# Optimization experiments

Hardware: AMD Instinct MI355X
Metric: run time of the kernel (lower is better)

Reference implementation:

```python
import jax, jax.numpy as jnp
import numpy as np

EPS = 1e-07


def _splat_one(inp, idx4, w4, n):
    # inp: [C1, N] weighted features for one batch element
    # idx4: [4, N] int32 flat target indices (clipped)
    # w4:  [4, N] bilinear weights (zeroed where out of bounds)
    out = jnp.zeros((inp.shape[0], n), dtype=inp.dtype)
    for k in range(4):
        out = out.at[:, idx4[k]].add(inp * w4[k])
    return out


def _softsplat(x, flow, metric):
    B, C, H, W = x.shape
    N = H * W
    m = jnp.exp(metric)                      # [B,1,H,W]
    inp = jnp.concatenate([x * m, m], axis=1)  # [B,C+1,H,W]

    gy, gx = jnp.meshgrid(jnp.arange(H, dtype=x.dtype),
                          jnp.arange(W, dtype=x.dtype), indexing='ij')
    tx = gx[None] + flow[:, 0]               # [B,H,W] target x
    ty = gy[None] + flow[:, 1]               # [B,H,W] target y

    x0f = jnp.floor(tx)
    y0f = jnp.floor(ty)
    x0 = x0f.astype(jnp.int32)
    y0 = y0f.astype(jnp.int32)
    x1 = x0 + 1
    y1 = y0 + 1

    fx = tx - x0f                            # frac parts
    fy = ty - y0f
    # bilinear weights for (x0,y0),(x1,y0),(x0,y1),(x1,y1)
    w = jnp.stack([(1 - fx) * (1 - fy),
                   fx * (1 - fy),
                   (1 - fx) * fy,
                   fx * fy], axis=1)          # [B,4,H,W]
    xs = jnp.stack([x0, x1, x0, x1], axis=1)  # [B,4,H,W]
    ys = jnp.stack([y0, y0, y1, y1], axis=1)

    valid = (xs >= 0) & (xs < W) & (ys >= 0) & (ys < H)
    w = jnp.where(valid, w, 0.0).reshape(B, 4, N)
    idx = (jnp.clip(ys, 0, H - 1) * W + jnp.clip(xs, 0, W - 1)).reshape(B, 4, N)

    inp_flat = inp.reshape(B, C + 1, N)
    out = jax.vmap(lambda i, ix, ww: _splat_one(i, ix, ww, N))(inp_flat, idx, w)
    out = out.reshape(B, C + 1, H, W)
    return out[:, :-1] / (out[:, -1:] + EPS)


def setup_inputs() -> dict:
    key = jax.random.key(0)
    k1, k2, k3 = jax.random.split(key, 3)
    x = jax.random.normal(k1, (8, 64, 256, 448), dtype=jnp.float32)
    flow = jax.random.normal(k2, (8, 2, 256, 448), dtype=jnp.float32)
    metric = jax.random.normal(k3, (8, 1, 256, 448), dtype=jnp.float32)
    return {"x": x, "flow": flow, "metric": metric}


def reference(x, flow, metric):
    return _softsplat(x, flow, metric)
```

## Files before the change

kernel.cpp:

```cpp
#include <hip/hip_runtime.h>

#define EPS 1e-7f

constexpr int B = 8, C = 64, H = 256, W = 448;
constexpr int N = H * W;
constexpr int P = B * N;

constexpr int TS  = 16;
constexpr int NT  = 256;
constexpr int RW  = 8;
constexpr int WIN = 32;
constexpr int NW  = WIN * WIN;
constexpr int TGS = 40;
constexpr int K   = 15;
constexpr int CHB = 8;
constexpr int NCHUNK = C / CHB;
constexpr float FMAX = 7.0f;
constexpr int TX = W / TS, TY = H / TS;
constexpr int TILES = B * TX * TY;
constexpr int NXCD = 8;

constexpr int L_TGT = 0, L_FX = 1280, L_FY = 2304, L_EM = 3328, L_PK = 4352;
constexpr int LDS_WORDS = 8192;

typedef __fp16 h2_t __attribute__((ext_vector_type(2)));
static __device__ __forceinline__ unsigned pk2(float a, float b) {
    h2_t h = __builtin_amdgcn_cvt_pkrtz(a, b);
    return __builtin_bit_cast(unsigned, h);
}
static __device__ __forceinline__ float2 up2(unsigned u) {
    h2_t h = __builtin_bit_cast(h2_t, u);
    return make_float2((float)h.x, (float)h.y);
}

__device__ int g_flag;

__global__ void zero_flag_k() { g_flag = 0; }

__global__ __launch_bounds__(256) void flag_scan(const float* __restrict__ flow)
{
    int t = blockIdx.x * blockDim.x + threadIdx.x;
    if (t >= P) return;
    int b = t / N, p = t - b * N;
    float fdx = flow[(size_t)(b * 2 + 0) * N + p];
    float fdy = flow[(size_t)(b * 2 + 1) * N + p];
    if (fabsf(fdx) > FMAX || fabsf(fdy) > FMAX) atomicAdd(&g_flag, 1);
}

#define STAGE_LOAD(gg)                                                        \
    {                                                                         \
        const int cbase = (gg) * CHB;                                         \
        const int row = tid >> 3;                                             \
        const int sc0 = (tid & 7) * 4;                                        \
        const int sh = ty0 - RW + row;                                        \
        const int sc = tx0 - RW + sc0;                                        \
        const bool v = (sh >= 0) & (sh < H) & (sc >= 0) & (sc < W);           \
        const float* bp = xb + (sh * W + sc);                                 \
        _Pragma("unroll")                                                     \
        for (int ch = 0; ch < CHB; ++ch)                                      \
            fr[ch] = v ? *(const float4*)(bp + (size_t)(cbase + ch) * N)      \
                       : make_float4(0.f, 0.f, 0.f, 0.f);                     \
    }

#define STAGE_WRITE(bufsel)                                                   \
    {                                                                         \
        char* base = (char*)lds + (bufsel) * 16384;                           \
        _Pragma("unroll")                                                     \
        for (int k = 0; k < 4; ++k) {                                         \
            const unsigned pos = 4u * (unsigned)tid + (unsigned)k;            \
            const unsigned blk = pos ^ ((pos >> 3) & 7u);                     \
            uint4 wv;                                                         \
            wv.x = pk2(((const float*)&fr[0])[k], ((const float*)&fr[1])[k]); \
            wv.y = pk2(((const float*)&fr[2])[k], ((const float*)&fr[3])[k]); \
            wv.z = pk2(((const float*)&fr[4])[k], ((const float*)&fr[5])[k]); \
            wv.w = pk2(((const float*)&fr[6])[k], ((const float*)&fr[7])[k]); \
            *(uint4*)(base + blk * 16) = wv;                                  \
        }                                                                     \
    }

__global__ __launch_bounds__(NT) void softsplat_fused(
    const float* __restrict__ x,
    const float* __restrict__ flow,
    const float* __restrict__ metric,
    float* __restrict__ out,
    float* __restrict__ den)
{
    __shared__ float lds[LDS_WORDS];
    unsigned* s_tgt = (unsigned*)(lds + L_TGT);
    float*    s_fx  = lds + L_FX;
    float*    s_fy  = lds + L_FY;
    float*    s_em  = lds + L_EM;
    unsigned* s_pk  = (unsigned*)(lds + L_PK);

    int bid = blockIdx.x;
    bid = (bid % NXCD) * (TILES / NXCD) + bid / NXCD;

    const int b   = bid / (TX * TY);
    const int tp  = bid % (TX * TY);
    const int ty0 = (tp / TX) * TS;
    const int tx0 = (tp % TX) * TS;
    const int tid = threadIdx.x;

    const float* fxg = flow + (size_t)(b * 2 + 0) * N;
    const float* fyg = flow + (size_t)(b * 2 + 1) * N;
    const float* mg  = metric + (size_t)b * N;

    float mymax = 0.f;
    for (int i = tid; i < NW; i += NT) {
        const int wy = i >> 5, wx = i & 31;
        const int sh = ty0 - RW + wy, sw = tx0 - RW + wx;
        unsigned t = 0xFFFFFFFFu;
        if (sh >= 0 && sh < H && sw >= 0 && sw < W) {
            const int sp = sh * W + sw;
            const float a = fxg[sp], bb = fyg[sp];
            if (fabsf(a) <= FMAX && fabsf(bb) <= FMAX) {
                const float xf = floorf(a), yf = floorf(bb);
                const int tx0g = sw + (int)xf + 16;
                const int ty0g = sh + (int)yf + 16;
                t = ((unsigned)ty0g << 16) | (unsigned)tx0g;
                s_fx[i] = a - xf;
                s_fy[i] = bb - yf;
                s_em[i] = __expf(mg[sp]);
                mymax = fmaxf(mymax, fmaxf(fabsf(a), fabsf(bb)));
            }
        }
        s_tgt[wy * TGS + wx] = t;
    }
    #pragma unroll
    for (int m = 1; m < 64; m <<= 1) mymax = fmaxf(mymax, __shfl_xor(mymax, m));
    if ((tid & 63) == 0) lds[L_PK + (tid >> 6)] = mymax;
    __syncthreads();
    const float M = fmaxf(fmaxf(lds[L_PK + 0], lds[L_PK + 1]),
                          fmaxf(lds[L_PK + 2], lds[L_PK + 3]));
    const int Rdyn = min(RW, (int)M + 1);
    __syncthreads();

    const int qxl = tid & (TS - 1), qyl = tid >> 4;
    const int qx = tx0 + qxl, qy = ty0 + qyl;
    const int q  = qy * W + qx;
    const unsigned qx16 = (unsigned)(qx + 16), qy16 = (unsigned)(qy + 16);

    int cnt = 0;
    float dacc = 0.f;
    for (int dy = -Rdyn; dy <= Rdyn; ++dy) {
        const int lrow = qyl + RW + dy;
        const int trow = lrow * TGS + (qxl + RW);
        for (int dx = -Rdyn; dx <= Rdyn; ++dx) {
            const unsigned t = s_tgt[trow + dx];
            const unsigned du = qx16 - (t & 0xFFFFu);
            const unsigned dv = qy16 - (t >> 16);
            if (max(du, dv) > 1u) continue;
            const int fi = lrow * WIN + (qxl + RW + dx);
            const float fxf = s_fx[fi], fyf = s_fy[fi];
            const float wxf = du ? fxf : 1.f - fxf;
            const float wyf = dv ? fyf : 1.f - fyf;
            const float w = wxf * wyf * s_em[fi];
            if (cnt < K)
                s_pk[cnt * NT + tid] = (__float_as_uint(w) & 0xFFFFFC00u) | (unsigned)fi;
            cnt++;
            dacc += w;
        }
    }
    for (int j = cnt; j < K; ++j)
        s_pk[j * NT + tid] = (unsigned)((qyl + RW) * WIN + (qxl + RW));

    int km = cnt;
    #pragma unroll
    for (int m = 1; m < 64; m <<= 1) km = max(km, __shfl_xor(km, m));
    const int kwave = min(K, __builtin_amdgcn_readfirstlane(km));

    const int flag = g_flag;
    const float rn = (flag == 0) ? 1.f / (dacc + EPS) : 1.f;

    const float* xb = x + (size_t)b * C * N;
    float* ob = out + (size_t)b * C * N + q;
    den[(size_t)b * N + q] = dacc;

    unsigned rsp[K]; float rw_[K];
    #pragma unroll
    for (int j = 0; j < K; ++j) {
        const unsigned pk = s_pk[j * NT + tid];
        const unsigned pos = pk & 0x3FFu;
        rsp[j] = (pos ^ ((pos >> 3) & 7u)) << 4;
        rw_[j] = __uint_as_float(pk & 0xFFFFFC00u) * rn;
    }

    const bool ovf = (cnt > K);
    if (ovf) {
        for (int c = 0; c < C; ++c) {
            const float* xp = xb + (size_t)c * N;
            float a = 0.f;
            for (int dy = -Rdyn; dy <= Rdyn; ++dy) {
                const int lrow = qyl + RW + dy;
                const int trow = lrow * TGS + (qxl + RW);
                for (int dx = -Rdyn; dx <= Rdyn; ++dx) {
                    const unsigned t = s_tgt[trow + dx];
                    const unsigned du = qx16 - (t & 0xFFFFu);
                    const unsigned dv = qy16 - (t >> 16);
                    if (max(du, dv) > 1u) continue;
                    const int fi = lrow * WIN + (qxl + RW + dx);
                    const float fxf = s_fx[fi], fyf = s_fy[fi];
                    const float wxf = du ? fxf : 1.f - fxf;
                    const float wyf = dv ? fyf : 1.f - fyf;
                    a = fmaf(wxf * wyf * s_em[fi], xp[(qy + dy) * W + (qx + dx)], a);
                }
            }
            ob[(size_t)c * N] = a * rn;
        }
    }
    __syncthreads();

    float4 fr[CHB];
    STAGE_LOAD(0)
    STAGE_WRITE(0)
    __syncthreads();
    for (int g = 0; g < NCHUNK; ++g) {
        const char* bc = (const char*)lds + (g & 1) * 16384;
        if (g + 1 < NCHUNK) STAGE_LOAD(g + 1)
        float a0 = 0.f, a1 = 0.f, a2 = 0.f, a3 = 0.f;
        float a4 = 0.f, a5 = 0.f, a6 = 0.f, a7 = 0.f;
        #pragma unroll
        for (int j = 0; j < K; ++j) {
            if (j >= kwave) break;
            const uint4 v = *(const uint4*)(bc + rsp[j]);
            const float wj = rw_[j];
            float2 p;
            p = up2(v.x); a0 = fmaf(wj, p.x, a0); a1 = fmaf(wj, p.y, a1);
            p = up2(v.y); a2 = fmaf(wj, p.x, a2); a3 = fmaf(wj, p.y, a3);
            p = up2(v.z); a4 = fmaf(wj, p.x, a4); a5 = fmaf(wj, p.y, a5);
            p = up2(v.w); a6 = fmaf(wj, p.x, a6); a7 = fmaf(wj, p.y, a7);
        }
        if (!ovf) {
            ob[(size_t)(g * CHB + 0) * N] = a0;
            ob[(size_t)(g * CHB + 1) * N] = a1;
            ob[(size_t)(g * CHB + 2) * N] = a2;
            ob[(size_t)(g * CHB + 3) * N] = a3;
            ob[(size_t)(g * CHB + 4) * N] = a4;
            ob[(size_t)(g * CHB + 5) * N] = a5;
            ob[(size_t)(g * CHB + 6) * N] = a6;
            ob[(size_t)(g * CHB + 7) * N] = a7;
        }
        if (g + 1 < NCHUNK) STAGE_WRITE((g & 1) ^ 1)
        __syncthreads();
    }
}

__global__ __launch_bounds__(256) void softsplat_outlier(
    const float* __restrict__ x,
    const float* __restrict__ flow,
    const float* __restrict__ metric,
    float* __restrict__ out,
    float* __restrict__ den)
{
    int t = blockIdx.x * blockDim.x + threadIdx.x;
    if (t >= P) return;
    int b = t / N;
    int p = t - b * N;
    float fdx = flow[(size_t)(b * 2 + 0) * N + p];
    float fdy = flow[(size_t)(b * 2 + 1) * N + p];
    if (fabsf(fdx) <= FMAX && fabsf(fdy) <= FMAX) return;

    int h = p / W, w = p - h * W;
    float m = __expf(metric[(size_t)b * N + p]);
    float tx = (float)w + fdx, ty = (float)h + fdy;
    float x0f = floorf(tx), y0f = floorf(ty);
    int x0 = (int)x0f, y0 = (int)y0f, x1 = x0 + 1, y1 = y0 + 1;
    float fx = tx - x0f, fy = ty - y0f;
    float w00 = (1.f - fx) * (1.f - fy), w10 = fx * (1.f - fy);
    float w01 = (1.f - fx) * fy,         w11 = fx * fy;
    bool vx0 = (x0 >= 0) && (x0 < W), vx1 = (x1 >= 0) && (x1 < W);
    bool vy0 = (y0 >= 0) && (y0 < H), vy1 = (y1 >= 0) && (y1 < H);
    int cx0 = min(max(x0, 0), W - 1), cx1 = min(max(x1, 0), W - 1);
    int cy0 = min(max(y0, 0), H - 1), cy1 = min(max(y1, 0), H - 1);
    int i00 = cy0 * W + cx0, i10 = cy0 * W + cx1;
    int i01 = cy1 * W + cx0, i11 = cy1 * W + cx1;
    w00 = (vx0 && vy0) ? w00 * m : 0.f;
    w10 = (vx1 && vy0) ? w10 * m : 0.f;
    w01 = (vx0 && vy1) ? w01 * m : 0.f;
    w11 = (vx1 && vy1) ? w11 * m : 0.f;

    float* denb = den + (size_t)b * N;
    if (w00 != 0.f) atomicAdd(denb + i00, w00);
    if (w10 != 0.f) atomicAdd(denb + i10, w10);
    if (w01 != 0.f) atomicAdd(denb + i01, w01);
    if (w11 != 0.f) atomicAdd(denb + i11, w11);

    const float* xb = x + (size_t)b * C * N + p;
    float* ob = out + (size_t)b * C * N;
    for (int c = 0; c < C; ++c) {
        float v = xb[(size_t)c * N];
        float* o = ob + (size_t)c * N;
        if (w00 != 0.f) atomicAdd(o + i00, v * w00);
        if (w10 != 0.f) atomicAdd(o + i10, v * w10);
        if (w01 != 0.f) atomicAdd(o + i01, v * w01);
        if (w11 != 0.f) atomicAdd(o + i11, v * w11);
    }
}

__global__ __launch_bounds__(256) void softsplat_norm(
    float* __restrict__ out, const float* __restrict__ den)
{
    if (g_flag == 0) return;
    size_t t = (size_t)blockIdx.x * blockDim.x + threadIdx.x;
    size_t e = t * 4;
    if (e >= (size_t)B * C * N) return;
    size_t b = e / ((size_t)C * N);
    size_t p = (e - b * (size_t)C * N) % N;

    float4 o = *reinterpret_cast<float4*>(out + e);
    const float4 d = *reinterpret_cast<const float4*>(den + b * N + p);
    o.x = o.x / (d.x + EPS);
    o.y = o.y / (d.y + EPS);
    o.z = o.z / (d.z + EPS);
    o.w = o.w / (d.w + EPS);
    *reinterpret_cast<float4*>(out + e) = o;
}

extern "C" void kernel_launch(void* const* d_in, const int* in_sizes, int n_in,
                              void* d_out, int out_size, void* d_ws, size_t ws_size,
                              hipStream_t stream) {
    const float* x      = (const float*)d_in[0];
    const float* flow   = (const float*)d_in[1];
    const float* metric = (const float*)d_in[2];
    float* out = (float*)d_out;
    float* den = (float*)d_ws;

    zero_flag_k<<<1, 1, 0, stream>>>();
    flag_scan<<<(P + 255) / 256, 256, 0, stream>>>(flow);

    softsplat_fused<<<TILES, NT, 0, stream>>>(x, flow, metric, out, den);

    softsplat_outlier<<<(P + 255) / 256, 256, 0, stream>>>(x, flow, metric, out, den);

    size_t nvec4 = (size_t)B * C * N / 4;
    softsplat_norm<<<(int)((nvec4 + 255) / 256), 256, 0, stream>>>(out, den);
}
```

Measured before the change: 238.7 us.

## Deepen staging prefetch to two chunks and use per-axis search radii

The channel-chunk loop now keeps two register staging buffers, so global loads for a chunk are issued two iterations ahead of the LDS compute that uses them, and the loop is fully unrolled in pairs. Separately, the flow-magnitude max is reduced per axis, so the neighbourhood search uses independent x and y radii instead of one square radius. The aim is to hide more global-load latency and scan fewer candidate sources. The cost is a second set of staging registers, which raises register pressure and may lower occupancy.

New measurement: 240.3 us. Within noise of the previous version (+0.7%).

```diff
diff --git a/kernel.cpp b/kernel.cpp
--- a/kernel.cpp
+++ b/kernel.cpp
@@ -47,7 +47,7 @@
     if (fabsf(fdx) > FMAX || fabsf(fdy) > FMAX) atomicAdd(&g_flag, 1);
 }
 
-#define STAGE_LOAD(gg)                                                        \
+#define STAGE_LOAD(dst, gg)                                                   \
     {                                                                         \
         const int cbase = (gg) * CHB;                                         \
         const int row = tid >> 3;                                             \
@@ -58,11 +58,11 @@
         const float* bp = xb + (sh * W + sc);                                 \
         _Pragma("unroll")                                                     \
         for (int ch = 0; ch < CHB; ++ch)                                      \
-            fr[ch] = v ? *(const float4*)(bp + (size_t)(cbase + ch) * N)      \
-                       : make_float4(0.f, 0.f, 0.f, 0.f);                     \
-    }
-
-#define STAGE_WRITE(bufsel)                                                   \
+            dst[ch] = v ? *(const float4*)(bp + (size_t)(cbase + ch) * N)     \
+                        : make_float4(0.f, 0.f, 0.f, 0.f);                    \
+    }
+
+#define STAGE_WRITE(src, bufsel)                                              \
     {                                                                         \
         char* base = (char*)lds + (bufsel) * 16384;                           \
         _Pragma("unroll")                                                     \
@@ -70,11 +70,39 @@
             const unsigned pos = 4u * (unsigned)tid + (unsigned)k;            \
             const unsigned blk = pos ^ ((pos >> 3) & 7u);                     \
             uint4 wv;                                                         \
-            wv.x = pk2(((const float*)&fr[0])[k], ((const float*)&fr[1])[k]); \
-            wv.y = pk2(((const float*)&fr[2])[k], ((const float*)&fr[3])[k]); \
-            wv.z = pk2(((const float*)&fr[4])[k], ((const float*)&fr[5])[k]); \
-            wv.w = pk2(((const float*)&fr[6])[k], ((const float*)&fr[7])[k]); \
+            wv.x = pk2(((const float*)&src[0])[k], ((const float*)&src[1])[k]); \
+            wv.y = pk2(((const float*)&src[2])[k], ((const float*)&src[3])[k]); \
+            wv.z = pk2(((const float*)&src[4])[k], ((const float*)&src[5])[k]); \
+            wv.w = pk2(((const float*)&src[6])[k], ((const float*)&src[7])[k]); \
             *(uint4*)(base + blk * 16) = wv;                                  \
+        }                                                                     \
+    }
+
+#define COMPUTE_STORE(bufsel, gg)                                             \
+    {                                                                         \
+        const char* bc = (const char*)lds + (bufsel) * 16384;                 \
+        float a0 = 0.f, a1 = 0.f, a2 = 0.f, a3 = 0.f;                         \
+        float a4 = 0.f, a5 = 0.f, a6 = 0.f, a7 = 0.f;                         \
+        _Pragma("unroll")                                                     \
+        for (int j = 0; j < K; ++j) {                                         \
+            if (j >= kwave) break;                   \
+            const uint4 v = *(const uint4*)(bc + rsp[j]);                     \
+            const float wj = rw_[j];                                          \
+            float2 pp;                                                        \
+            pp = up2(v.x); a0 = fmaf(wj, pp.x, a0); a1 = fmaf(wj, pp.y, a1);  \
+            pp = up2(v.y); a2 = fmaf(wj, pp.x, a2); a3 = fmaf(wj, pp.y, a3);  \
+            pp = up2(v.z); a4 = fmaf(wj, pp.x, a4); a5 = fmaf(wj, pp.y, a5);  \
+            pp = up2(v.w); a6 = fmaf(wj, pp.x, a6); a7 = fmaf(wj, pp.y, a7);  \
+        }                                                                     \
+        if (!ovf) {                                                           \
+            ob[(size_t)((gg) * CHB + 0) * N] = a0;                            \
+            ob[(size_t)((gg) * CHB + 1) * N] = a1;                            \
+            ob[(size_t)((gg) * CHB + 2) * N] = a2;                            \
+            ob[(size_t)((gg) * CHB + 3) * N] = a3;                            \
+            ob[(size_t)((gg) * CHB + 4) * N] = a4;                            \
+            ob[(size_t)((gg) * CHB + 5) * N] = a5;                            \
+            ob[(size_t)((gg) * CHB + 6) * N] = a6;                            \
+            ob[(size_t)((gg) * CHB + 7) * N] = a7;                            \
         }                                                                     \
     }
 
@@ -105,7 +133,7 @@
     const float* fyg = flow + (size_t)(b * 2 + 1) * N;
     const float* mg  = metric + (size_t)b * N;
 
-    float mymax = 0.f;
+    float mxx = 0.f, mxy = 0.f;
     for (int i = tid; i < NW; i += NT) {
         const int wy = i >> 5, wx = i & 31;
         const int sh = ty0 - RW + wy, sw = tx0 - RW + wx;
@@ -121,18 +149,28 @@
                 s_fx[i] = a - xf;
                 s_fy[i] = bb - yf;
                 s_em[i] = __expf(mg[sp]);
-                mymax = fmaxf(mymax, fmaxf(fabsf(a), fabsf(bb)));
+                mxx = fmaxf(mxx, fabsf(a));
+                mxy = fmaxf(mxy, fabsf(bb));
             }
         }
         s_tgt[wy * TGS + wx] = t;
     }
     #pragma unroll
-    for (int m = 1; m < 64; m <<= 1) mymax = fmaxf(mymax, __shfl_xor(mymax, m));
-    if ((tid & 63) == 0) lds[L_PK + (tid >> 6)] = mymax;
+    for (int m = 1; m < 64; m <<= 1) {
+        mxx = fmaxf(mxx, __shfl_xor(mxx, m));
+        mxy = fmaxf(mxy, __shfl_xor(mxy, m));
+    }
+    if ((tid & 63) == 0) {
+        lds[L_PK + 2 * (tid >> 6) + 0] = mxx;
+        lds[L_PK + 2 * (tid >> 6) + 1] = mxy;
+    }
     __syncthreads();
-    const float M = fmaxf(fmaxf(lds[L_PK + 0], lds[L_PK + 1]),
-                          fmaxf(lds[L_PK + 2], lds[L_PK + 3]));
-    const int Rdyn = min(RW, (int)M + 1);
+    const float Mx = fmaxf(fmaxf(lds[L_PK + 0], lds[L_PK + 2]),
+                           fmaxf(lds[L_PK + 4], lds[L_PK + 6]));
+    const float My = fmaxf(fmaxf(lds[L_PK + 1], lds[L_PK + 3]),
+                           fmaxf(lds[L_PK + 5], lds[L_PK + 7]));
+    const int Rx = min(RW, (int)Mx + 1);
+    const int Ry = min(RW, (int)My + 1);
     __syncthreads();
 
     const int qxl = tid & (TS - 1), qyl = tid >> 4;
@@ -142,10 +180,10 @@
 
     int cnt = 0;
     float dacc = 0.f;
-    for (int dy = -Rdyn; dy <= Rdyn; ++dy) {
+    for (int dy = -Ry; dy <= Ry; ++dy) {
         const int lrow = qyl + RW + dy;
         const int trow = lrow * TGS + (qxl + RW);
-        for (int dx = -Rdyn; dx <= Rdyn; ++dx) {
+        for (int dx = -Rx; dx <= Rx; ++dx) {
             const unsigned t = s_tgt[trow + dx];
             const unsigned du = qx16 - (t & 0xFFFFu);
             const unsigned dv = qy16 - (t >> 16);
@@ -190,10 +228,10 @@
         for (int c = 0; c < C; ++c) {
             const float* xp = xb + (size_t)c * N;
             float a = 0.f;
-            for (int dy = -Rdyn; dy <= Rdyn; ++dy) {
+            for (int dy = -Ry; dy <= Ry; ++dy) {
                 const int lrow = qyl + RW + dy;
                 const int trow = lrow * TGS + (qxl + RW);
-                for (int dx = -Rdyn; dx <= Rdyn; ++dx) {
+                for (int dx = -Rx; dx <= Rx; ++dx) {
                     const unsigned t = s_tgt[trow + dx];
                     const unsigned du = qx16 - (t & 0xFFFFu);
                     const unsigned dv = qy16 - (t >> 16);
@@ -210,37 +248,20 @@
     }
     __syncthreads();
 
-    float4 fr[CHB];
-    STAGE_LOAD(0)
-    STAGE_WRITE(0)
+    float4 fr0[CHB], fr1[CHB];
+    STAGE_LOAD(fr0, 0)
+    STAGE_WRITE(fr0, 0)
+    STAGE_LOAD(fr1, 1)
     __syncthreads();
-    for (int g = 0; g < NCHUNK; ++g) {
-        const char* bc = (const char*)lds + (g & 1) * 16384;
-        if (g + 1 < NCHUNK) STAGE_LOAD(g + 1)
-        float a0 = 0.f, a1 = 0.f, a2 = 0.f, a3 = 0.f;
-        float a4 = 0.f, a5 = 0.f, a6 = 0.f, a7 = 0.f;
-        #pragma unroll
-        for (int j = 0; j < K; ++j) {
-            if (j >= kwave) break;
-            const uint4 v = *(const uint4*)(bc + rsp[j]);
-            const float wj = rw_[j];
-            float2 p;
-            p = up2(v.x); a0 = fmaf(wj, p.x, a0); a1 = fmaf(wj, p.y, a1);
-            p = up2(v.y); a2 = fmaf(wj, p.x, a2); a3 = fmaf(wj, p.y, a3);
-            p = up2(v.z); a4 = fmaf(wj, p.x, a4); a5 = fmaf(wj, p.y, a5);
-            p = up2(v.w); a6 = fmaf(wj, p.x, a6); a7 = fmaf(wj, p.y, a7);
-        }
-        if (!ovf) {
-            ob[(size_t)(g * CHB + 0) * N] = a0;
-            ob[(size_t)(g * CHB + 1) * N] = a1;
-            ob[(size_t)(g * CHB + 2) * N] = a2;
-            ob[(size_t)(g * CHB + 3) * N] = a3;
-            ob[(size_t)(g * CHB + 4) * N] = a4;
-            ob[(size_t)(g * CHB + 5) * N] = a5;
-            ob[(size_t)(g * CHB + 6) * N] = a6;
-            ob[(size_t)(g * CHB + 7) * N] = a7;
-        }
-        if (g + 1 < NCHUNK) STAGE_WRITE((g & 1) ^ 1)
+    #pragma unroll
+    for (int gp = 0; gp < NCHUNK; gp += 2) {
+        if (gp + 2 < NCHUNK) STAGE_LOAD(fr0, gp + 2)
+        COMPUTE_STORE(0, gp)
+        STAGE_WRITE(fr1, 1)
+        __syncthreads();
+        if (gp + 3 < NCHUNK) STAGE_LOAD(fr1, gp + 3)
+        COMPUTE_STORE(1, gp + 1)
+        if (gp + 2 < NCHUNK) STAGE_WRITE(fr0, 0)
         __syncthreads();
     }
 }
```
